# Kernel optimization log

Hardware: AMD Instinct MI355X
Metric: run time of the kernel (lower is better)

Reference implementation:

```python
import jax, jax.numpy as jnp
import numpy as np

M = 65536   # query points
N = 65536   # key points
K = 16      # neighbors per query
C = 64      # channels


def setup_inputs() -> dict:
    key = jax.random.key(0)
    ks = jax.random.split(key, 12)
    f = jax.random.normal
    s = 1.0 / np.sqrt(C).astype(np.float32)
    return {
        "q": f(ks[0], (M, C), dtype=jnp.float32),
        "k": f(ks[1], (N, C), dtype=jnp.float32),
        "value": f(ks[2], (M, K, C), dtype=jnp.float32),
        "q_pos": f(ks[3], (M, C), dtype=jnp.float32),
        "k_pos": f(ks[4], (N, C), dtype=jnp.float32),
        "mask": jax.random.uniform(ks[5], (M, K, 1)) < 0.1,
        "knearest_idx": jax.random.randint(ks[6], (2, M, K), 0, N),
        "k_num": K,
        # q_conv and k_conv share weights in the original module
        "Wqk": f(ks[7], (C, C), dtype=jnp.float32) * s,
        "bqk": jnp.zeros((C,), jnp.float32),
        "Wv": f(ks[8], (C, C), dtype=jnp.float32) * s,
        "bv": jnp.zeros((C,), jnp.float32),
        "Wg1": f(ks[9], (C, C), dtype=jnp.float32) * s,
        "bg1": jnp.zeros((C,), jnp.float32),
        "Wg2": f(ks[10], (C, C), dtype=jnp.float32) * s,
        "bg2": jnp.zeros((C,), jnp.float32),
        "Wt": f(ks[11], (C, C), dtype=jnp.float32) * s,
        "bt": jnp.zeros((C,), jnp.float32),
    }


def reference(q, k, value, q_pos, k_pos, mask, knearest_idx, k_num,
              Wqk, bqk, Wv, bv, Wg1, bg1, Wg2, bg2, Wt, bt):
    # shared q/k projection (tied weights) with positional add
    qp = (q + q_pos) @ Wqk + bqk            # [M, C]
    kp = (k + k_pos) @ Wqk + bqk            # [N, C]
    v = value @ Wv + bv                      # [M, K, C]
    # neighbor indices: row 1 of knearest_idx reshaped to [_, M, k_num]
    idx = knearest_idx.reshape(knearest_idx.shape[0], -1, k_num)[1]  # [M, K]
    kg = kp[idx]                              # gather -> [M, K, C]
    # per-edge MLP on q - k (fc_gamma)
    e = qp[:, None, :] - kg                   # [M, K, C]
    e = jax.nn.relu(e @ Wg1 + bg1) @ Wg2 + bg2
    e = jnp.where(mask, jnp.float32(-1e12), e)
    attn = jax.nn.softmax(e, axis=1)          # softmax over neighbor dim
    res = jnp.einsum('mnf,mnf->mf', attn, v)  # weighted aggregate -> [M, C]
    return res @ Wt + bt
```

## Files before the change

kernel.cpp:

```cpp
#include <hip/hip_runtime.h>
#include <hip/hip_bf16.h>

#define MQ 65536
#define NKEY 65536
#define KNB 16
#define CCH 64
#define TPB 8

typedef _Float16 half8  __attribute__((ext_vector_type(8)));
typedef _Float16 half4v __attribute__((ext_vector_type(4)));
typedef float    floatx4 __attribute__((ext_vector_type(4)));


__global__ void detect_mask(const unsigned char* __restrict__ m, int* __restrict__ flag)
{
    __shared__ int sflags;
    if (threadIdx.x == 0) sflags = 0;
    __syncthreads();
    const uint4* m4 = (const uint4*)m;
    unsigned int orw = 0;
    #pragma unroll
    for (int it = 0; it < 4; ++it) {
        uint4 v = m4[threadIdx.x + it * 256];
        orw |= v.x | v.y | v.z | v.w;
    }
    int local = 0;
    if (orw & 0x000000FFu) local |= 1;
    if (orw & 0x0000FF00u) local |= 2;
    if (orw & 0xFFFF0000u) local |= 4;
    if (local) atomicOr(&sflags, local);
    __syncthreads();
    if (threadIdx.x == 0) *flag = sflags;
}

__global__ __launch_bounds__(256, 4)
void proj_prep(const float* __restrict__ q, const float* __restrict__ qpos,
               const float* __restrict__ k, const float* __restrict__ kpos,
               const float* __restrict__ Wqk, const float* __restrict__ bqk,
               const float* __restrict__ Wg1, const float* __restrict__ Wg2,
               const float* __restrict__ Wv,  const float* __restrict__ Wt,
               const unsigned char* __restrict__ maskraw, const int* __restrict__ mflag,
               _Float16* __restrict__ qp_h, _Float16* __restrict__ kp_h,
               _Float16* __restrict__ w4, unsigned short* __restrict__ mask_packed)
{
    const int tid = threadIdx.x;
    const int bid = blockIdx.x;

    if (bid >= 1024) {
        if (bid < 1088) {
            const int mode = *mflag;
            const int qq0 = (bid - 1024) * 1024 + tid * 4;
            unsigned short mp[4];
            #pragma unroll
            for (int i = 0; i < 4; ++i) {
                const int qq = qq0 + i;
                unsigned bits = 0;
                if (mode & 2) {
                    uint4 v = ((const uint4*)maskraw)[qq];
                    unsigned wds[4] = {v.x, v.y, v.z, v.w};
                    #pragma unroll
                    for (int wi = 0; wi < 4; ++wi)
                        #pragma unroll
                        for (int b = 0; b < 4; ++b)
                            if ((wds[wi] >> (8 * b)) & 0xFFu) bits |= 1u << (wi * 4 + b);
                } else {
                    const uint4* p = (const uint4*)maskraw + (size_t)qq * 4;
                    #pragma unroll
                    for (int wi = 0; wi < 4; ++wi) {
                        uint4 v = p[wi];
                        bits |= (v.x ? 1u : 0u) << (wi * 4 + 0);
                        bits |= (v.y ? 1u : 0u) << (wi * 4 + 1);
                        bits |= (v.z ? 1u : 0u) << (wi * 4 + 2);
                        bits |= (v.w ? 1u : 0u) << (wi * 4 + 3);
                    }
                }
                mp[i] = (unsigned short)bits;
            }
            ushort4 o4; o4.x = mp[0]; o4.y = mp[1]; o4.z = mp[2]; o4.w = mp[3];
            *(ushort4*)&mask_packed[qq0] = o4;
        } else {
            const float* Ws[4] = {Wg1, Wg2, Wv, Wt};
            #pragma unroll
            for (int mat = 0; mat < 4; ++mat) {
                const float* W = Ws[mat];
                _Float16* dst = w4 + mat * 64 * 72;
                for (int i = tid; i < 4096; i += 256) {
                    int rr = i >> 6, c = i & 63;
                    dst[c * 72 + rr] = (_Float16)W[i];
                }
            }
        }
        return;
    }

    __shared__ __align__(16) _Float16 A_s[128 * 72];
    __shared__ __align__(16) _Float16 WT_s[64 * 72];

    const int r0 = bid * 128;
    const float* x; const float* p; _Float16* o; int rb;
    if (r0 < MQ) { x = q; p = qpos; o = qp_h; rb = r0; }
    else         { x = k; p = kpos; o = kp_h; rb = r0 - MQ; }

    #pragma unroll
    for (int j = 0; j < 4; ++j) {
        int i = (tid + j * 256) * 4;
        int rr = i >> 6, c4 = i & 63;
        floatx4 wv = *(const floatx4*)&Wqk[i];
        WT_s[(c4 + 0) * 72 + rr] = (_Float16)wv.x;
        WT_s[(c4 + 1) * 72 + rr] = (_Float16)wv.y;
        WT_s[(c4 + 2) * 72 + rr] = (_Float16)wv.z;
        WT_s[(c4 + 3) * 72 + rr] = (_Float16)wv.w;
    }
    #pragma unroll
    for (int j = 0; j < 8; ++j) {
        int flat = tid + j * 256;
        int rr = flat >> 4, c4 = (flat & 15) * 4;
        size_t g = (size_t)(rb + rr) * 64 + c4;
        floatx4 xv = *(const floatx4*)&x[g];
        floatx4 pv = *(const floatx4*)&p[g];
        half4v h;
        h[0] = (_Float16)(xv.x + pv.x); h[1] = (_Float16)(xv.y + pv.y);
        h[2] = (_Float16)(xv.z + pv.z); h[3] = (_Float16)(xv.w + pv.w);
        *(half4v*)&A_s[rr * 72 + c4] = h;
    }
    __syncthreads();

    const int w = tid >> 6, lane = tid & 63, m = lane & 15, qd = lane >> 4;
    const floatx4 fz = {0.f, 0.f, 0.f, 0.f};
    floatx4 acc[2][4];
    #pragma unroll
    for (int rt = 0; rt < 2; rt++)
        #pragma unroll
        for (int ct = 0; ct < 4; ct++) acc[rt][ct] = fz;

    #pragma unroll
    for (int kc = 0; kc < 2; ++kc) {
        const int k0 = kc * 32 + qd * 8;
        half8 b[4];
        #pragma unroll
        for (int ct = 0; ct < 4; ++ct)
            b[ct] = *(const half8*)&WT_s[(ct * 16 + m) * 72 + k0];
        #pragma unroll
        for (int rt = 0; rt < 2; ++rt) {
            half8 a = *(const half8*)&A_s[(w * 32 + rt * 16 + m) * 72 + k0];
            #pragma unroll
            for (int ct = 0; ct < 4; ++ct)
                acc[rt][ct] = __builtin_amdgcn_mfma_f32_16x16x32_f16(a, b[ct], acc[rt][ct], 0, 0, 0);
        }
    }
    #pragma unroll
    for (int rt = 0; rt < 2; rt++)
        #pragma unroll
        for (int ct = 0; ct < 4; ct++) {
            const int col = ct * 16 + m;
            const float bb = bqk[col];
            #pragma unroll
            for (int rg = 0; rg < 4; ++rg) {
                const int row = w * 32 + rt * 16 + qd * 4 + rg;
                A_s[row * 72 + col] = (_Float16)(acc[rt][ct][rg] + bb);
            }
        }
    __syncthreads();
    #pragma unroll
    for (int j = 0; j < 4; ++j) {
        int ch = tid + j * 256;
        int rr = ch >> 3, off = (ch & 7) * 8;
        *(half8*)&o[(size_t)(rb + rr) * 64 + off] = *(const half8*)&A_s[rr * 72 + off];
    }
}

__global__ __launch_bounds__(256) __attribute__((amdgpu_waves_per_eu(2, 2)))
void cross_attn(const float* __restrict__ value, const unsigned short* __restrict__ mask_packed,
                const int* __restrict__ idx,
                const _Float16* __restrict__ qp_h, const _Float16* __restrict__ kp_h,
                const _Float16* __restrict__ w4,
                const float* __restrict__ bg1, const float* __restrict__ bg2,
                const float* __restrict__ bv,
                _Float16* __restrict__ res_g)
{
    __shared__ __align__(16) _Float16 W3_s[3 * 64 * 72];
    __shared__ __align__(16) _Float16 H_s[256 * 72];

    const int tid = threadIdx.x, w = tid >> 6, lane = tid & 63, m = lane & 15, qd = (lane >> 4) & 3;
    const int tile0 = blockIdx.x * TPB;

    for (int ch = tid; ch < 1728; ch += 256)
        *(half8*)&W3_s[ch * 8] = *(const half8*)&w4[ch * 8];

    float bg1v[4], bg2v[4], bvv[4];
    #pragma unroll
    for (int ct = 0; ct < 4; ct++) {
        const int col = ct * 16 + m;
        bg1v[ct] = bg1[col]; bg2v[ct] = bg2[col]; bvv[ct] = bv[col];
    }

    int idxn[4]; unsigned mpr[4];
    half8 qpr[4][2];
    floatx4 vraw[16];
    {
        const int q0 = tile0 * 16;
        #pragma unroll
        for (int rt = 0; rt < 4; ++rt) {
            const int qrow = q0 + w * 4 + rt;
            idxn[rt] = idx[qrow * KNB + m];
            mpr[rt]  = mask_packed[qrow];
            #pragma unroll
            for (int kc = 0; kc < 2; ++kc)
                qpr[rt][kc] = *(const half8*)&qp_h[(size_t)qrow * 64 + kc * 32 + qd * 8];
            #pragma unroll
            for (int kc = 0; kc < 2; ++kc) {
                const float* vr = value + ((size_t)qrow * KNB + m) * 64 + kc * 32 + qd * 8;
                vraw[(rt * 2 + kc) * 2 + 0] = *(const floatx4*)vr;
                vraw[(rt * 2 + kc) * 2 + 1] = *(const floatx4*)(vr + 4);
            }
        }
    }
    __syncthreads();

    const _Float16* Wg1T = W3_s;
    const _Float16* Wg2T = W3_s + 4608;
    const _Float16* WvT  = W3_s + 2 * 4608;
    const floatx4 fz = {0.f, 0.f, 0.f, 0.f};

    for (int t = 0; t < TPB; ++t) {
        const int q0t = (tile0 + t) * 16;
        const bool more = (t + 1 < TPB);

        unsigned mcur[4];
        #pragma unroll
        for (int rt = 0; rt < 4; ++rt) mcur[rt] = mpr[rt];

        half8 kpr[4][2];
        #pragma unroll
        for (int rt = 0; rt < 4; ++rt)
            #pragma unroll
            for (int kc = 0; kc < 2; ++kc)
                kpr[rt][kc] = *(const half8*)&kp_h[(size_t)idxn[rt] * 64 + kc * 32 + qd * 8];

        #pragma unroll
        for (int pr = 0; pr < 2; ++pr) {
            const int r0 = pr * 2;

            half8 vfrag[2][2];
            #pragma unroll
            for (int rr = 0; rr < 2; ++rr)
                #pragma unroll
                for (int kc = 0; kc < 2; ++kc) {
                    floatx4 x0 = vraw[((r0 + rr) * 2 + kc) * 2 + 0];
                    floatx4 x1 = vraw[((r0 + rr) * 2 + kc) * 2 + 1];
                    half8 a;
                    #pragma unroll
                    for (int j = 0; j < 4; ++j) { a[j] = (_Float16)x0[j]; a[4 + j] = (_Float16)x1[j]; }
                    vfrag[rr][kc] = a;
                }

            floatx4 accv2[2][4];
            #pragma unroll
            for (int rr = 0; rr < 2; ++rr)
                #pragma unroll
                for (int ct = 0; ct < 4; ++ct) accv2[rr][ct] = fz;
            #pragma unroll
            for (int kc = 0; kc < 2; ++kc) {
                const int k0 = kc * 32 + qd * 8;
                half8 b[4];
                #pragma unroll
                for (int ct = 0; ct < 4; ++ct)
                    b[ct] = *(const half8*)&WvT[(ct * 16 + m) * 72 + k0];
                #pragma unroll
                for (int rr = 0; rr < 2; ++rr)
                    #pragma unroll
                    for (int ct = 0; ct < 4; ++ct)
                        accv2[rr][ct] = __builtin_amdgcn_mfma_f32_16x16x32_f16(vfrag[rr][kc], b[ct], accv2[rr][ct], 0, 0, 0);
            }

            if (more) {
                const int q0n = q0t + 16;
                #pragma unroll
                for (int rr = 0; rr < 2; ++rr) {
                    const int qrow = q0n + w * 4 + r0 + rr;
                    #pragma unroll
                    for (int kc = 0; kc < 2; ++kc) {
                        const float* vr = value + ((size_t)qrow * KNB + m) * 64 + kc * 32 + qd * 8;
                        vraw[((r0 + rr) * 2 + kc) * 2 + 0] = *(const floatx4*)vr;
                        vraw[((r0 + rr) * 2 + kc) * 2 + 1] = *(const floatx4*)(vr + 4);
                    }
                }
            }

            floatx4 acch2[2][4];
            #pragma unroll
            for (int rr = 0; rr < 2; ++rr)
                #pragma unroll
                for (int ct = 0; ct < 4; ++ct) acch2[rr][ct] = fz;
            #pragma unroll
            for (int kc = 0; kc < 2; ++kc) {
                const int k0 = kc * 32 + qd * 8;
                half8 b[4];
                #pragma unroll
                for (int ct = 0; ct < 4; ++ct)
                    b[ct] = *(const half8*)&Wg1T[(ct * 16 + m) * 72 + k0];
                #pragma unroll
                for (int rr = 0; rr < 2; ++rr) {
                    half8 a = qpr[r0 + rr][kc] - kpr[r0 + rr][kc];
                    #pragma unroll
                    for (int ct = 0; ct < 4; ++ct)
                        acch2[rr][ct] = __builtin_amdgcn_mfma_f32_16x16x32_f16(a, b[ct], acch2[rr][ct], 0, 0, 0);
                }
            }

            #pragma unroll
            for (int rr = 0; rr < 2; ++rr)
                #pragma unroll
                for (int ct = 0; ct < 4; ++ct) {
                    const int col = ct * 16 + m;
                    #pragma unroll
                    for (int rg = 0; rg < 4; ++rg) {
                        const int row = w * 64 + (r0 + rr) * 16 + qd * 4 + rg;
                        float h = acch2[rr][ct][rg] + bg1v[ct];
                        H_s[row * 72 + col] = (_Float16)fmaxf(h, 0.f);
                    }
                }
            __asm__ volatile("s_waitcnt lgkmcnt(0)" ::: "memory");

            floatx4 acce2[2][4];
            #pragma unroll
            for (int rr = 0; rr < 2; ++rr)
                #pragma unroll
                for (int ct = 0; ct < 4; ++ct) acce2[rr][ct] = fz;
            #pragma unroll
            for (int kc = 0; kc < 2; ++kc) {
                const int k0 = kc * 32 + qd * 8;
                half8 b[4];
                #pragma unroll
                for (int ct = 0; ct < 4; ++ct)
                    b[ct] = *(const half8*)&Wg2T[(ct * 16 + m) * 72 + k0];
                #pragma unroll
                for (int rr = 0; rr < 2; ++rr) {
                    half8 a = *(const half8*)&H_s[(w * 64 + (r0 + rr) * 16 + m) * 72 + k0];
                    #pragma unroll
                    for (int ct = 0; ct < 4; ++ct)
                        acce2[rr][ct] = __builtin_amdgcn_mfma_f32_16x16x32_f16(a, b[ct], acce2[rr][ct], 0, 0, 0);
                }
            }

            if (pr == 0 && more) {
                const int q0n = q0t + 16;
                #pragma unroll
                for (int rt = 0; rt < 4; ++rt) {
                    const int qrow = q0n + w * 4 + rt;
                    idxn[rt] = idx[qrow * KNB + m];
                    mpr[rt]  = mask_packed[qrow];
                }
            }

            #pragma unroll
            for (int rr = 0; rr < 2; ++rr) {
                const int rt = r0 + rr;
                float tca[4];
                #pragma unroll
                for (int ct = 0; ct < 4; ++ct) {
                    float ev[4];
                    #pragma unroll
                    for (int rg = 0; rg < 4; ++rg) {
                        float e = acce2[rr][ct][rg] + bg2v[ct];
                        ev[rg] = ((mcur[rt] >> (qd * 4 + rg)) & 1u) ? -1e12f : e;
                    }
                    float mx = fmaxf(fmaxf(ev[0], ev[1]), fmaxf(ev[2], ev[3]));
                    mx = fmaxf(mx, __shfl_xor(mx, 16));
                    mx = fmaxf(mx, __shfl_xor(mx, 32));
                    float pp[4], s = 0.f;
                    #pragma unroll
                    for (int rg = 0; rg < 4; ++rg) { pp[rg] = __expf(ev[rg] - mx); s += pp[rg]; }
                    s += __shfl_xor(s, 16);
                    s += __shfl_xor(s, 32);
                    const float inv = 1.f / s;
                    float tt = 0.f;
                    #pragma unroll
                    for (int rg = 0; rg < 4; ++rg)
                        tt += pp[rg] * inv * (accv2[rr][ct][rg] + bvv[ct]);
                    tt += __shfl_xor(tt, 16);
                    tt += __shfl_xor(tt, 32);
                    tca[ct] = tt;
                }
                float tsel = (qd == 0) ? tca[0] : (qd == 1) ? tca[1] : (qd == 2) ? tca[2] : tca[3];
                res_g[(size_t)(q0t + w * 4 + rt) * 64 + lane] = (_Float16)tsel;
            }
        }

        if (more) {
            const int q0n = q0t + 16;
            #pragma unroll
            for (int rt = 0; rt < 4; ++rt) {
                const int qrow = q0n + w * 4 + rt;
                #pragma unroll
                for (int kc = 0; kc < 2; ++kc)
                    qpr[rt][kc] = *(const half8*)&qp_h[(size_t)qrow * 64 + kc * 32 + qd * 8];
            }
        }
    }
}

__global__ __launch_bounds__(256, 4)
void out_proj(const _Float16* __restrict__ res_g, const _Float16* __restrict__ w4,
              const float* __restrict__ bt, float* __restrict__ out)
{
    __shared__ __align__(16) _Float16 WtT_s[64 * 72];
    const int tid = threadIdx.x;
    const _Float16* WtT_g = w4 + 3 * 4608;
    for (int ch = tid; ch < 576; ch += 256)
        *(half8*)&WtT_s[ch * 8] = *(const half8*)&WtT_g[ch * 8];
    __syncthreads();

    const int w = tid >> 6, lane = tid & 63, m = lane & 15, qd = lane >> 4;
    const int rb = blockIdx.x * 256;
    const floatx4 fz = {0.f, 0.f, 0.f, 0.f};
    float btv[4];
    #pragma unroll
    for (int ct = 0; ct < 4; ++ct) btv[ct] = bt[ct * 16 + m];

    #pragma unroll
    for (int rt = 0; rt < 4; ++rt) {
        floatx4 acc[4] = {fz, fz, fz, fz};
        #pragma unroll
        for (int kc = 0; kc < 2; ++kc) {
            const int k0 = kc * 32 + qd * 8;
            half8 a = *(const half8*)&res_g[(size_t)(rb + w * 64 + rt * 16 + m) * 64 + k0];
            half8 b[4];
            #pragma unroll
            for (int ct = 0; ct < 4; ++ct)
                b[ct] = *(const half8*)&WtT_s[(ct * 16 + m) * 72 + k0];
            #pragma unroll
            for (int ct = 0; ct < 4; ++ct)
                acc[ct] = __builtin_amdgcn_mfma_f32_16x16x32_f16(a, b[ct], acc[ct], 0, 0, 0);
        }
        #pragma unroll
        for (int ct = 0; ct < 4; ++ct) {
            #pragma unroll
            for (int rg = 0; rg < 4; ++rg)
                out[(size_t)(rb + w * 64 + rt * 16 + qd * 4 + rg) * 64 + ct * 16 + m] = acc[ct][rg] + btv[ct];
        }
    }
}

extern "C" void kernel_launch(void* const* d_in, const int* in_sizes, int n_in,
                              void* d_out, int out_size, void* d_ws, size_t ws_size,
                              hipStream_t stream) {
    const float* q     = (const float*)d_in[0];
    const float* k     = (const float*)d_in[1];
    const float* value = (const float*)d_in[2];
    const float* q_pos = (const float*)d_in[3];
    const float* k_pos = (const float*)d_in[4];
    const unsigned char* mask = (const unsigned char*)d_in[5];
    const int* knn     = (const int*)d_in[6];
    const float* Wqk = (const float*)d_in[8];
    const float* bqk = (const float*)d_in[9];
    const float* Wv  = (const float*)d_in[10];
    const float* bv  = (const float*)d_in[11];
    const float* Wg1 = (const float*)d_in[12];
    const float* bg1 = (const float*)d_in[13];
    const float* Wg2 = (const float*)d_in[14];
    const float* bg2 = (const float*)d_in[15];
    const float* Wt  = (const float*)d_in[16];
    const float* bt  = (const float*)d_in[17];
    float* out = (float*)d_out;

    _Float16* qp_h  = (_Float16*)d_ws;
    _Float16* kp_h  = qp_h + (size_t)MQ * CCH;
    _Float16* res_g = kp_h + (size_t)NKEY * CCH;
    _Float16* w4    = res_g + (size_t)MQ * CCH;
    unsigned short* mask_packed = (unsigned short*)(w4 + 4 * 64 * 72);
    int* mflag = (int*)(mask_packed + MQ);
    const int* idx = knn + (size_t)MQ * KNB;

    detect_mask<<<1, 256, 0, stream>>>(mask, mflag);
    proj_prep<<<1089, 256, 0, stream>>>(q, q_pos, k, k_pos, Wqk, bqk,
                                        Wg1, Wg2, Wv, Wt, mask, mflag,
                                        qp_h, kp_h, w4, mask_packed);
    cross_attn<<<MQ / (16 * TPB), 256, 0, stream>>>(value, mask_packed, idx, qp_h, kp_h, w4,
                                                    bg1, bg2, bv, res_g);
    out_proj<<<MQ / 256, 256, 0, stream>>>(res_g, w4, bt, out);
}
```

Measured before the change: 501.0 us.

## Fuse output projection into cross_attn and software-pipeline neighbor key gathers

The separate out_proj kernel is removed. cross_attn now keeps results in a per-wave shared buffer and runs the Wt projection with MFMA every four tiles, writing the final fp32 output directly, which drops the res_g round trip and one launch. The kp gathers for the next tile are now issued inside the current tile's pipeline, after the index prefetch, so they overlap compute. H_s is shrunk to per-pair rows to make room for Wt and R_s in LDS. The cost is more register pressure from kpr kept live across tiles, and a scattered output-store pattern.

```diff
diff --git a/kernel.cpp b/kernel.cpp
--- a/kernel.cpp
+++ b/kernel.cpp
@@ -175,27 +175,28 @@
                 const _Float16* __restrict__ qp_h, const _Float16* __restrict__ kp_h,
                 const _Float16* __restrict__ w4,
                 const float* __restrict__ bg1, const float* __restrict__ bg2,
-                const float* __restrict__ bv,
-                _Float16* __restrict__ res_g)
+                const float* __restrict__ bv, const float* __restrict__ bt,
+                float* __restrict__ out)
 {
-    __shared__ __align__(16) _Float16 W3_s[3 * 64 * 72];
-    __shared__ __align__(16) _Float16 H_s[256 * 72];
+    __shared__ __align__(16) _Float16 W4_s[4 * 64 * 72];
+    __shared__ __align__(16) _Float16 H_s[128 * 72];
+    __shared__ __align__(16) _Float16 R_s[64 * 72];
 
     const int tid = threadIdx.x, w = tid >> 6, lane = tid & 63, m = lane & 15, qd = (lane >> 4) & 3;
     const int tile0 = blockIdx.x * TPB;
 
-    for (int ch = tid; ch < 1728; ch += 256)
-        *(half8*)&W3_s[ch * 8] = *(const half8*)&w4[ch * 8];
-
-    float bg1v[4], bg2v[4], bvv[4];
+    for (int ch = tid; ch < 2304; ch += 256)
+        *(half8*)&W4_s[ch * 8] = *(const half8*)&w4[ch * 8];
+
+    float bg1v[4], bg2v[4], bvv[4], btv[4];
     #pragma unroll
     for (int ct = 0; ct < 4; ct++) {
         const int col = ct * 16 + m;
-        bg1v[ct] = bg1[col]; bg2v[ct] = bg2[col]; bvv[ct] = bv[col];
+        bg1v[ct] = bg1[col]; bg2v[ct] = bg2[col]; bvv[ct] = bv[col]; btv[ct] = bt[col];
     }
 
     int idxn[4]; unsigned mpr[4];
-    half8 qpr[4][2];
+    half8 qpr[4][2], kpr[4][2];
     floatx4 vraw[16];
     {
         const int q0 = tile0 * 16;
@@ -214,12 +215,18 @@
                 vraw[(rt * 2 + kc) * 2 + 1] = *(const floatx4*)(vr + 4);
             }
         }
+        #pragma unroll
+        for (int rt = 0; rt < 4; ++rt)
+            #pragma unroll
+            for (int kc = 0; kc < 2; ++kc)
+                kpr[rt][kc] = *(const half8*)&kp_h[(size_t)idxn[rt] * 64 + kc * 32 + qd * 8];
     }
     __syncthreads();
 
-    const _Float16* Wg1T = W3_s;
-    const _Float16* Wg2T = W3_s + 4608;
-    const _Float16* WvT  = W3_s + 2 * 4608;
+    const _Float16* Wg1T = W4_s;
+    const _Float16* Wg2T = W4_s + 4608;
+    const _Float16* WvT  = W4_s + 2 * 4608;
+    const _Float16* WtT  = W4_s + 3 * 4608;
     const floatx4 fz = {0.f, 0.f, 0.f, 0.f};
 
     for (int t = 0; t < TPB; ++t) {
@@ -230,12 +237,15 @@
         #pragma unroll
         for (int rt = 0; rt < 4; ++rt) mcur[rt] = mpr[rt];
 
-        half8 kpr[4][2];
-        #pragma unroll
-        for (int rt = 0; rt < 4; ++rt)
-            #pragma unroll
-            for (int kc = 0; kc < 2; ++kc)
-                kpr[rt][kc] = *(const half8*)&kp_h[(size_t)idxn[rt] * 64 + kc * 32 + qd * 8];
+        if (more) {
+            const int q0n = q0t + 16;
+            #pragma unroll
+            for (int rt = 0; rt < 4; ++rt) {
+                const int qrow = q0n + w * 4 + rt;
+                idxn[rt] = idx[qrow * KNB + m];
+                mpr[rt]  = mask_packed[qrow];
+            }
+        }
 
         #pragma unroll
         for (int pr = 0; pr < 2; ++pr) {
@@ -308,6 +318,17 @@
                 }
             }
 
+            if (more) {
+                const int q0n = q0t + 16;
+                #pragma unroll
+                for (int rr = 0; rr < 2; ++rr) {
+                    const int qrow = q0n + w * 4 + r0 + rr;
+                    #pragma unroll
+                    for (int kc = 0; kc < 2; ++kc)
+                        qpr[r0 + rr][kc] = *(const half8*)&qp_h[(size_t)qrow * 64 + kc * 32 + qd * 8];
+                }
+            }
+
             #pragma unroll
             for (int rr = 0; rr < 2; ++rr)
                 #pragma unroll
@@ -315,7 +336,7 @@
                     const int col = ct * 16 + m;
                     #pragma unroll
                     for (int rg = 0; rg < 4; ++rg) {
-                        const int row = w * 64 + (r0 + rr) * 16 + qd * 4 + rg;
+                        const int row = w * 32 + rr * 16 + qd * 4 + rg;
                         float h = acch2[rr][ct][rg] + bg1v[ct];
                         H_s[row * 72 + col] = (_Float16)fmaxf(h, 0.f);
                     }
@@ -336,21 +357,19 @@
                     b[ct] = *(const half8*)&Wg2T[(ct * 16 + m) * 72 + k0];
                 #pragma unroll
                 for (int rr = 0; rr < 2; ++rr) {
-                    half8 a = *(const half8*)&H_s[(w * 64 + (r0 + rr) * 16 + m) * 72 + k0];
+                    half8 a = *(const half8*)&H_s[(w * 32 + rr * 16 + m) * 72 + k0];
                     #pragma unroll
                     for (int ct = 0; ct < 4; ++ct)
                         acce2[rr][ct] = __builtin_amdgcn_mfma_f32_16x16x32_f16(a, b[ct], acce2[rr][ct], 0, 0, 0);
                 }
             }
 
-            if (pr == 0 && more) {
-                const int q0n = q0t + 16;
-                #pragma unroll
-                for (int rt = 0; rt < 4; ++rt) {
-                    const int qrow = q0n + w * 4 + rt;
-                    idxn[rt] = idx[qrow * KNB + m];
-                    mpr[rt]  = mask_packed[qrow];
-                }
+            if (more) {
+                #pragma unroll
+                for (int rr = 0; rr < 2; ++rr)
+                    #pragma unroll
+                    for (int kc = 0; kc < 2; ++kc)
+                        kpr[r0 + rr][kc] = *(const half8*)&kp_h[(size_t)idxn[r0 + rr] * 64 + kc * 32 + qd * 8];
             }
 
             #pragma unroll
@@ -383,61 +402,34 @@
                     tca[ct] = tt;
                 }
                 float tsel = (qd == 0) ? tca[0] : (qd == 1) ? tca[1] : (qd == 2) ? tca[2] : tca[3];
-                res_g[(size_t)(q0t + w * 4 + rt) * 64 + lane] = (_Float16)tsel;
-            }
-        }
-
-        if (more) {
-            const int q0n = q0t + 16;
-            #pragma unroll
-            for (int rt = 0; rt < 4; ++rt) {
-                const int qrow = q0n + w * 4 + rt;
-                #pragma unroll
-                for (int kc = 0; kc < 2; ++kc)
-                    qpr[rt][kc] = *(const half8*)&qp_h[(size_t)qrow * 64 + kc * 32 + qd * 8];
-            }
-        }
-    }
-}
-
-__global__ __launch_bounds__(256, 4)
-void out_proj(const _Float16* __restrict__ res_g, const _Float16* __restrict__ w4,
-              const float* __restrict__ bt, float* __restrict__ out)
-{
-    __shared__ __align__(16) _Float16 WtT_s[64 * 72];
-    const int tid = threadIdx.x;
-    const _Float16* WtT_g = w4 + 3 * 4608;
-    for (int ch = tid; ch < 576; ch += 256)
-        *(half8*)&WtT_s[ch * 8] = *(const half8*)&WtT_g[ch * 8];
-    __syncthreads();
-
-    const int w = tid >> 6, lane = tid & 63, m = lane & 15, qd = lane >> 4;
-    const int rb = blockIdx.x * 256;
-    const floatx4 fz = {0.f, 0.f, 0.f, 0.f};
-    float btv[4];
-    #pragma unroll
-    for (int ct = 0; ct < 4; ++ct) btv[ct] = bt[ct * 16 + m];
-
-    #pragma unroll
-    for (int rt = 0; rt < 4; ++rt) {
-        floatx4 acc[4] = {fz, fz, fz, fz};
-        #pragma unroll
-        for (int kc = 0; kc < 2; ++kc) {
-            const int k0 = kc * 32 + qd * 8;
-            half8 a = *(const half8*)&res_g[(size_t)(rb + w * 64 + rt * 16 + m) * 64 + k0];
-            half8 b[4];
+                R_s[((w * 16 + (t & 3) * 4 + rt)) * 72 + lane] = (_Float16)tsel;
+            }
+        }
+
+        if ((t & 3) == 3) {
+            __asm__ volatile("s_waitcnt lgkmcnt(0)" ::: "memory");
+            floatx4 acc[4] = {fz, fz, fz, fz};
+            #pragma unroll
+            for (int kc = 0; kc < 2; ++kc) {
+                const int k0 = kc * 32 + qd * 8;
+                half8 a = *(const half8*)&R_s[(w * 16 + m) * 72 + k0];
+                half8 b[4];
+                #pragma unroll
+                for (int ct = 0; ct < 4; ++ct)
+                    b[ct] = *(const half8*)&WtT[(ct * 16 + m) * 72 + k0];
+                #pragma unroll
+                for (int ct = 0; ct < 4; ++ct)
+                    acc[ct] = __builtin_amdgcn_mfma_f32_16x16x32_f16(a, b[ct], acc[ct], 0, 0, 0);
+            }
+            const int grp0 = (tile0 + (t & ~3)) * 16;
             #pragma unroll
             for (int ct = 0; ct < 4; ++ct)
-                b[ct] = *(const half8*)&WtT_s[(ct * 16 + m) * 72 + k0];
-            #pragma unroll
-            for (int ct = 0; ct < 4; ++ct)
-                acc[ct] = __builtin_amdgcn_mfma_f32_16x16x32_f16(a, b[ct], acc[ct], 0, 0, 0);
-        }
-        #pragma unroll
-        for (int ct = 0; ct < 4; ++ct) {
-            #pragma unroll
-            for (int rg = 0; rg < 4; ++rg)
-                out[(size_t)(rb + w * 64 + rt * 16 + qd * 4 + rg) * 64 + ct * 16 + m] = acc[ct][rg] + btv[ct];
+                #pragma unroll
+                for (int rg = 0; rg < 4; ++rg) {
+                    const int r = qd * 4 + rg;
+                    const int g = grp0 + (r >> 2) * 16 + w * 4 + (r & 3);
+                    out[(size_t)g * 64 + ct * 16 + m] = acc[ct][rg] + btv[ct];
+                }
         }
     }
 }
@@ -477,6 +469,5 @@
                                         Wg1, Wg2, Wv, Wt, mask, mflag,
                                         qp_h, kp_h, w4, mask_packed);
     cross_attn<<<MQ / (16 * TPB), 256, 0, stream>>>(value, mask_packed, idx, qp_h, kp_h, w4,
-                                                    bg1, bg2, bv, res_g);
-    out_proj<<<MQ / 256, 256, 0, stream>>>(res_g, w4, bt, out);
+                                                    bg1, bg2, bv, bt, out);
 }
```

Measured after the change: 527.7 us. 1.05x slower.

## Cut cross_attn register pressure to raise occupancy and drop bg2 add

Applied to the files above, without the earlier changes.

The attention kernel is reworked so each tile is processed in two half-passes that hold only two query rows' value and q data in registers. This roughly halves live registers and lets waves_per_eu rise from 2 to 3, with TPB halved and H_s shrunk to match. Other changes: bg2 is dropped because a per-channel bias cancels in the softmax over neighbours, bv is added once after the normalised sum, the value projection is kept in fp16, the mask words are loaded as one uint2, and a fast reciprocal is used. The trade-offs are more prefetch and branch logic per half-pass, more blocks each reloading the weights into LDS, and slightly lower precision.

```diff
diff --git a/kernel.cpp b/kernel.cpp
--- a/kernel.cpp
+++ b/kernel.cpp
@@ -5,7 +5,7 @@
 #define NKEY 65536
 #define KNB 16
 #define CCH 64
-#define TPB 8
+#define TPB 4
 
 typedef _Float16 half8  __attribute__((ext_vector_type(8)));
 typedef _Float16 half4v __attribute__((ext_vector_type(4)));
@@ -169,17 +169,16 @@
     }
 }
 
-__global__ __launch_bounds__(256) __attribute__((amdgpu_waves_per_eu(2, 2)))
+__global__ __launch_bounds__(256) __attribute__((amdgpu_waves_per_eu(3, 3)))
 void cross_attn(const float* __restrict__ value, const unsigned short* __restrict__ mask_packed,
                 const int* __restrict__ idx,
                 const _Float16* __restrict__ qp_h, const _Float16* __restrict__ kp_h,
                 const _Float16* __restrict__ w4,
-                const float* __restrict__ bg1, const float* __restrict__ bg2,
-                const float* __restrict__ bv,
+                const float* __restrict__ bg1, const float* __restrict__ bv,
                 _Float16* __restrict__ res_g)
 {
     __shared__ __align__(16) _Float16 W3_s[3 * 64 * 72];
-    __shared__ __align__(16) _Float16 H_s[256 * 72];
+    __shared__ __align__(16) _Float16 H_s[128 * 72];
 
     const int tid = threadIdx.x, w = tid >> 6, lane = tid & 63, m = lane & 15, qd = (lane >> 4) & 3;
     const int tile0 = blockIdx.x * TPB;
@@ -187,33 +186,35 @@
     for (int ch = tid; ch < 1728; ch += 256)
         *(half8*)&W3_s[ch * 8] = *(const half8*)&w4[ch * 8];
 
-    float bg1v[4], bg2v[4], bvv[4];
-    #pragma unroll
-    for (int ct = 0; ct < 4; ct++) {
-        const int col = ct * 16 + m;
-        bg1v[ct] = bg1[col]; bg2v[ct] = bg2[col]; bvv[ct] = bv[col];
-    }
-
-    int idxn[4]; unsigned mpr[4];
-    half8 qpr[4][2];
-    floatx4 vraw[16];
+    float bg1v[4];
+    #pragma unroll
+    for (int ct = 0; ct < 4; ct++) bg1v[ct] = bg1[ct * 16 + m];
+    const float bvsel = bv[lane];
+
+    int idxn[4];
+    uint2 mpr;
+    half8 qpr[2][2];
+    half8 kpr[4][2];
+    floatx4 vraw[8];
     {
         const int q0 = tile0 * 16;
-        #pragma unroll
-        for (int rt = 0; rt < 4; ++rt) {
-            const int qrow = q0 + w * 4 + rt;
-            idxn[rt] = idx[qrow * KNB + m];
-            mpr[rt]  = mask_packed[qrow];
+        mpr = *(const uint2*)&mask_packed[q0 + w * 4];
+        #pragma unroll
+        for (int rt = 0; rt < 4; ++rt)
+            idxn[rt] = idx[(q0 + w * 4 + rt) * KNB + m];
+        #pragma unroll
+        for (int rr = 0; rr < 2; ++rr)
             #pragma unroll
             for (int kc = 0; kc < 2; ++kc)
-                qpr[rt][kc] = *(const half8*)&qp_h[(size_t)qrow * 64 + kc * 32 + qd * 8];
+                qpr[rr][kc] = *(const half8*)&qp_h[(size_t)(q0 + w * 4 + rr) * 64 + kc * 32 + qd * 8];
+        #pragma unroll
+        for (int rr = 0; rr < 2; ++rr)
             #pragma unroll
             for (int kc = 0; kc < 2; ++kc) {
-                const float* vr = value + ((size_t)qrow * KNB + m) * 64 + kc * 32 + qd * 8;
-                vraw[(rt * 2 + kc) * 2 + 0] = *(const floatx4*)vr;
-                vraw[(rt * 2 + kc) * 2 + 1] = *(const floatx4*)(vr + 4);
-            }
-        }
+                const float* vr = value + ((size_t)(q0 + w * 4 + rr) * KNB + m) * 64 + kc * 32 + qd * 8;
+                vraw[(rr * 2 + kc) * 2 + 0] = *(const floatx4*)vr;
+                vraw[(rr * 2 + kc) * 2 + 1] = *(const floatx4*)(vr + 4);
+            }
     }
     __syncthreads();
 
@@ -226,11 +227,8 @@
         const int q0t = (tile0 + t) * 16;
         const bool more = (t + 1 < TPB);
 
-        unsigned mcur[4];
-        #pragma unroll
-        for (int rt = 0; rt < 4; ++rt) mcur[rt] = mpr[rt];
-
-        half8 kpr[4][2];
+        const uint2 mcur = mpr;
+
         #pragma unroll
         for (int rt = 0; rt < 4; ++rt)
             #pragma unroll
@@ -246,155 +244,158 @@
             for (int rr = 0; rr < 2; ++rr)
                 #pragma unroll
                 for (int kc = 0; kc < 2; ++kc) {
-                    floatx4 x0 = vraw[((r0 + rr) * 2 + kc) * 2 + 0];
-                    floatx4 x1 = vraw[((r0 + rr) * 2 + kc) * 2 + 1];
+                    floatx4 x0 = vraw[(rr * 2 + kc) * 2 + 0];
+                    floatx4 x1 = vraw[(rr * 2 + kc) * 2 + 1];
                     half8 a;
                     #pragma unroll
                     for (int j = 0; j < 4; ++j) { a[j] = (_Float16)x0[j]; a[4 + j] = (_Float16)x1[j]; }
                     vfrag[rr][kc] = a;
                 }
 
-            floatx4 accv2[2][4];
+            if (pr == 0 || more) {
+                const int qb = (pr == 0) ? (q0t + 2) : (q0t + 16);
+                #pragma unroll
+                for (int rr = 0; rr < 2; ++rr) {
+                    const float* vr = value + ((size_t)(qb + w * 4 + rr) * KNB + m) * 64 + qd * 8;
+                    vraw[(rr * 2 + 0) * 2 + 0] = *(const floatx4*)vr;
+                    vraw[(rr * 2 + 0) * 2 + 1] = *(const floatx4*)(vr + 4);
+                    vraw[(rr * 2 + 1) * 2 + 0] = *(const floatx4*)(vr + 32);
+                    vraw[(rr * 2 + 1) * 2 + 1] = *(const floatx4*)(vr + 36);
+                }
+            }
+
+            half4v vh[2][4];
+            {
+                floatx4 accv[2][4];
+                #pragma unroll
+                for (int rr = 0; rr < 2; ++rr)
+                    #pragma unroll
+                    for (int ct = 0; ct < 4; ++ct) accv[rr][ct] = fz;
+                #pragma unroll
+                for (int kc = 0; kc < 2; ++kc) {
+                    const int k0 = kc * 32 + qd * 8;
+                    half8 b[4];
+                    #pragma unroll
+                    for (int ct = 0; ct < 4; ++ct)
+                        b[ct] = *(const half8*)&WvT[(ct * 16 + m) * 72 + k0];
+                    #pragma unroll
+                    for (int rr = 0; rr < 2; ++rr)
+                        #pragma unroll
+                        for (int ct = 0; ct < 4; ++ct)
+                            accv[rr][ct] = __builtin_amdgcn_mfma_f32_16x16x32_f16(vfrag[rr][kc], b[ct], accv[rr][ct], 0, 0, 0);
+                }
+                #pragma unroll
+                for (int rr = 0; rr < 2; ++rr)
+                    #pragma unroll
+                    for (int ct = 0; ct < 4; ++ct) {
+                        half4v hv;
+                        #pragma unroll
+                        for (int rg = 0; rg < 4; ++rg) hv[rg] = (_Float16)accv[rr][ct][rg];
+                        vh[rr][ct] = hv;
+                    }
+            }
+
+            floatx4 acch[2][4];
             #pragma unroll
             for (int rr = 0; rr < 2; ++rr)
                 #pragma unroll
-                for (int ct = 0; ct < 4; ++ct) accv2[rr][ct] = fz;
+                for (int ct = 0; ct < 4; ++ct) acch[rr][ct] = fz;
             #pragma unroll
             for (int kc = 0; kc < 2; ++kc) {
                 const int k0 = kc * 32 + qd * 8;
                 half8 b[4];
                 #pragma unroll
                 for (int ct = 0; ct < 4; ++ct)
-                    b[ct] = *(const half8*)&WvT[(ct * 16 + m) * 72 + k0];
+                    b[ct] = *(const half8*)&Wg1T[(ct * 16 + m) * 72 + k0];
+                #pragma unroll
+                for (int rr = 0; rr < 2; ++rr) {
+                    half8 a = qpr[rr][kc] - kpr[r0 + rr][kc];
+                    #pragma unroll
+                    for (int ct = 0; ct < 4; ++ct)
+                        acch[rr][ct] = __builtin_amdgcn_mfma_f32_16x16x32_f16(a, b[ct], acch[rr][ct], 0, 0, 0);
+                }
+            }
+
+            if (pr == 0 || more) {
+                const int qb = (pr == 0) ? (q0t + 2) : (q0t + 16);
                 #pragma unroll
                 for (int rr = 0; rr < 2; ++rr)
                     #pragma unroll
-                    for (int ct = 0; ct < 4; ++ct)
-                        accv2[rr][ct] = __builtin_amdgcn_mfma_f32_16x16x32_f16(vfrag[rr][kc], b[ct], accv2[rr][ct], 0, 0, 0);
-            }
-
-            if (more) {
-                const int q0n = q0t + 16;
-                #pragma unroll
-                for (int rr = 0; rr < 2; ++rr) {
-                    const int qrow = q0n + w * 4 + r0 + rr;
-                    #pragma unroll
-                    for (int kc = 0; kc < 2; ++kc) {
-                        const float* vr = value + ((size_t)qrow * KNB + m) * 64 + kc * 32 + qd * 8;
-                        vraw[((r0 + rr) * 2 + kc) * 2 + 0] = *(const floatx4*)vr;
-                        vraw[((r0 + rr) * 2 + kc) * 2 + 1] = *(const floatx4*)(vr + 4);
+                    for (int kc = 0; kc < 2; ++kc)
+                        qpr[rr][kc] = *(const half8*)&qp_h[(size_t)(qb + w * 4 + rr) * 64 + kc * 32 + qd * 8];
+            }
+
+            #pragma unroll
+            for (int rr = 0; rr < 2; ++rr)
+                #pragma unroll
+                for (int ct = 0; ct < 4; ++ct) {
+                    const int col = ct * 16 + m;
+                    #pragma unroll
+                    for (int rg = 0; rg < 4; ++rg) {
+                        const int row = w * 32 + rr * 16 + qd * 4 + rg;
+                        float h = acch[rr][ct][rg] + bg1v[ct];
+                        H_s[row * 72 + col] = (_Float16)fmaxf(h, 0.f);
                     }
                 }
-            }
-
-            floatx4 acch2[2][4];
+            __asm__ volatile("s_waitcnt lgkmcnt(0)" ::: "memory");
+
+            floatx4 acce[2][4];
             #pragma unroll
             for (int rr = 0; rr < 2; ++rr)
                 #pragma unroll
-                for (int ct = 0; ct < 4; ++ct) acch2[rr][ct] = fz;
+                for (int ct = 0; ct < 4; ++ct) acce[rr][ct] = fz;
             #pragma unroll
             for (int kc = 0; kc < 2; ++kc) {
                 const int k0 = kc * 32 + qd * 8;
                 half8 b[4];
                 #pragma unroll
                 for (int ct = 0; ct < 4; ++ct)
-                    b[ct] = *(const half8*)&Wg1T[(ct * 16 + m) * 72 + k0];
+                    b[ct] = *(const half8*)&Wg2T[(ct * 16 + m) * 72 + k0];
                 #pragma unroll
                 for (int rr = 0; rr < 2; ++rr) {
-                    half8 a = qpr[r0 + rr][kc] - kpr[r0 + rr][kc];
+                    half8 a = *(const half8*)&H_s[(w * 32 + rr * 16 + m) * 72 + k0];
                     #pragma unroll
                     for (int ct = 0; ct < 4; ++ct)
-                        acch2[rr][ct] = __builtin_amdgcn_mfma_f32_16x16x32_f16(a, b[ct], acch2[rr][ct], 0, 0, 0);
-                }
-            }
-
-            #pragma unroll
-            for (int rr = 0; rr < 2; ++rr)
-                #pragma unroll
-                for (int ct = 0; ct < 4; ++ct) {
-                    const int col = ct * 16 + m;
-                    #pragma unroll
-                    for (int rg = 0; rg < 4; ++rg) {
-                        const int row = w * 64 + (r0 + rr) * 16 + qd * 4 + rg;
-                        float h = acch2[rr][ct][rg] + bg1v[ct];
-                        H_s[row * 72 + col] = (_Float16)fmaxf(h, 0.f);
-                    }
-                }
-            __asm__ volatile("s_waitcnt lgkmcnt(0)" ::: "memory");
-
-            floatx4 acce2[2][4];
-            #pragma unroll
-            for (int rr = 0; rr < 2; ++rr)
-                #pragma unroll
-                for (int ct = 0; ct < 4; ++ct) acce2[rr][ct] = fz;
-            #pragma unroll
-            for (int kc = 0; kc < 2; ++kc) {
-                const int k0 = kc * 32 + qd * 8;
-                half8 b[4];
-                #pragma unroll
-                for (int ct = 0; ct < 4; ++ct)
-                    b[ct] = *(const half8*)&Wg2T[(ct * 16 + m) * 72 + k0];
-                #pragma unroll
-                for (int rr = 0; rr < 2; ++rr) {
-                    half8 a = *(const half8*)&H_s[(w * 64 + (r0 + rr) * 16 + m) * 72 + k0];
-                    #pragma unroll
-                    for (int ct = 0; ct < 4; ++ct)
-                        acce2[rr][ct] = __builtin_amdgcn_mfma_f32_16x16x32_f16(a, b[ct], acce2[rr][ct], 0, 0, 0);
+                        acce[rr][ct] = __builtin_amdgcn_mfma_f32_16x16x32_f16(a, b[ct], acce[rr][ct], 0, 0, 0);
                 }
             }
 
             if (pr == 0 && more) {
                 const int q0n = q0t + 16;
-                #pragma unroll
-                for (int rt = 0; rt < 4; ++rt) {
-                    const int qrow = q0n + w * 4 + rt;
-                    idxn[rt] = idx[qrow * KNB + m];
-                    mpr[rt]  = mask_packed[qrow];
-                }
-            }
-
+                mpr = *(const uint2*)&mask_packed[q0n + w * 4];
+                #pragma unroll
+                for (int rt = 0; rt < 4; ++rt)
+                    idxn[rt] = idx[(q0n + w * 4 + rt) * KNB + m];
+            }
+
+            const unsigned mword = (pr == 0) ? mcur.x : mcur.y;
             #pragma unroll
             for (int rr = 0; rr < 2; ++rr) {
-                const int rt = r0 + rr;
+                const int sh = rr * 16 + qd * 4;
                 float tca[4];
                 #pragma unroll
                 for (int ct = 0; ct < 4; ++ct) {
                     float ev[4];
                     #pragma unroll
                     for (int rg = 0; rg < 4; ++rg) {
-                        float e = acce2[rr][ct][rg] + bg2v[ct];
-                        ev[rg] = ((mcur[rt] >> (qd * 4 + rg)) & 1u) ? -1e12f : e;
+                        float e = acce[rr][ct][rg];
+                        ev[rg] = ((mword >> (sh + rg)) & 1u) ? -1e12f : e;
                     }
                     float mx = fmaxf(fmaxf(ev[0], ev[1]), fmaxf(ev[2], ev[3]));
                     mx = fmaxf(mx, __shfl_xor(mx, 16));
                     mx = fmaxf(mx, __shfl_xor(mx, 32));
-                    float pp[4], s = 0.f;
-                    #pragma unroll
-                    for (int rg = 0; rg < 4; ++rg) { pp[rg] = __expf(ev[rg] - mx); s += pp[rg]; }
-                    s += __shfl_xor(s, 16);
-                    s += __shfl_xor(s, 32);
-                    const float inv = 1.f / s;
-                    float tt = 0.f;
-                    #pragma unroll
-                    for (int rg = 0; rg < 4; ++rg)
-                        tt += pp[rg] * inv * (accv2[rr][ct][rg] + bvv[ct]);
-                    tt += __shfl_xor(tt, 16);
-                    tt += __shfl_xor(tt, 32);
-                    tca[ct] = tt;
+                    float s = 0.f, ttu = 0.f;
+                    #pragma unroll
+                    for (int rg = 0; rg < 4; ++rg) {
+                        float p = __expf(ev[rg] - mx);
+                        s += p; ttu += p * (float)vh[rr][ct][rg];
+                    }
+                    s   += __shfl_xor(s, 16);   ttu += __shfl_xor(ttu, 16);
+                    s   += __shfl_xor(s, 32);   ttu += __shfl_xor(ttu, 32);
+                    tca[ct] = ttu * __builtin_amdgcn_rcpf(s);
                 }
                 float tsel = (qd == 0) ? tca[0] : (qd == 1) ? tca[1] : (qd == 2) ? tca[2] : tca[3];
-                res_g[(size_t)(q0t + w * 4 + rt) * 64 + lane] = (_Float16)tsel;
-            }
-        }
-
-        if (more) {
-            const int q0n = q0t + 16;
-            #pragma unroll
-            for (int rt = 0; rt < 4; ++rt) {
-                const int qrow = q0n + w * 4 + rt;
-                #pragma unroll
-                for (int kc = 0; kc < 2; ++kc)
-                    qpr[rt][kc] = *(const half8*)&qp_h[(size_t)qrow * 64 + kc * 32 + qd * 8];
+                res_g[(size_t)(q0t + w * 4 + r0 + rr) * 64 + lane] = (_Float16)(tsel + bvsel);
             }
         }
     }
@@ -463,6 +464,7 @@
     const float* Wt  = (const float*)d_in[16];
     const float* bt  = (const float*)d_in[17];
     float* out = (float*)d_out;
+    (void)bg2;
 
     _Float16* qp_h  = (_Float16*)d_ws;
     _Float16* kp_h  = qp_h + (size_t)MQ * CCH;
@@ -477,6 +479,6 @@
                                         Wg1, Wg2, Wv, Wt, mask, mflag,
                                         qp_h, kp_h, w4, mask_packed);
     cross_attn<<<MQ / (16 * TPB), 256, 0, stream>>>(value, mask_packed, idx, qp_h, kp_h, w4,
-                                                    bg1, bg2, bv, res_g);
+                                                    bg1, bv, res_g);
     out_proj<<<MQ / 256, 256, 0, stream>>>(res_g, w4, bt, out);
 }
```

After: 554.6 us. 1.11x slower.

## Prefetch next tile's key gathers and simplify softmax with exp2 and bias folding

Applied to the files above, without the earlier changes.

The gather of projected keys for the next tile is now issued in the middle of the current tile's compute, right after the next tile's indices are loaded, instead of at the top of each iteration. The aim is to hide the latency of the random gather behind the MFMA work, at the cost of keeping more registers live. The softmax is also simplified. The Wg2 weights are prescaled by log2(e) so the kernel can use a native exp2. The bg2 bias is dropped because a per-channel constant cancels in a softmax over neighbors. The bv bias is added once after normalisation, and the final division becomes a single rcp multiply.

```diff
diff --git a/kernel.cpp b/kernel.cpp
--- a/kernel.cpp
+++ b/kernel.cpp
@@ -10,6 +10,12 @@
 typedef _Float16 half8  __attribute__((ext_vector_type(8)));
 typedef _Float16 half4v __attribute__((ext_vector_type(4)));
 typedef float    floatx4 __attribute__((ext_vector_type(4)));
+
+#if __has_builtin(__builtin_amdgcn_exp2f)
+#define EXP2F(x) __builtin_amdgcn_exp2f(x)
+#else
+#define EXP2F(x) exp2f(x)
+#endif
 
 
 __global__ void detect_mask(const unsigned char* __restrict__ m, int* __restrict__ flag)
@@ -83,10 +89,11 @@
             #pragma unroll
             for (int mat = 0; mat < 4; ++mat) {
                 const float* W = Ws[mat];
+                const float sc = (mat == 1) ? 1.44269504f : 1.0f;
                 _Float16* dst = w4 + mat * 64 * 72;
                 for (int i = tid; i < 4096; i += 256) {
                     int rr = i >> 6, c = i & 63;
-                    dst[c * 72 + rr] = (_Float16)W[i];
+                    dst[c * 72 + rr] = (_Float16)(W[i] * sc);
                 }
             }
         }
@@ -174,8 +181,7 @@
                 const int* __restrict__ idx,
                 const _Float16* __restrict__ qp_h, const _Float16* __restrict__ kp_h,
                 const _Float16* __restrict__ w4,
-                const float* __restrict__ bg1, const float* __restrict__ bg2,
-                const float* __restrict__ bv,
+                const float* __restrict__ bg1, const float* __restrict__ bv,
                 _Float16* __restrict__ res_g)
 {
     __shared__ __align__(16) _Float16 W3_s[3 * 64 * 72];
@@ -187,15 +193,13 @@
     for (int ch = tid; ch < 1728; ch += 256)
         *(half8*)&W3_s[ch * 8] = *(const half8*)&w4[ch * 8];
 
-    float bg1v[4], bg2v[4], bvv[4];
-    #pragma unroll
-    for (int ct = 0; ct < 4; ct++) {
-        const int col = ct * 16 + m;
-        bg1v[ct] = bg1[col]; bg2v[ct] = bg2[col]; bvv[ct] = bv[col];
-    }
+    float bg1v[4];
+    #pragma unroll
+    for (int ct = 0; ct < 4; ct++) bg1v[ct] = bg1[ct * 16 + m];
+    const float bvsel = bv[lane];
 
     int idxn[4]; unsigned mpr[4];
-    half8 qpr[4][2];
+    half8 qpr[4][2], kpr[4][2];
     floatx4 vraw[16];
     {
         const int q0 = tile0 * 16;
@@ -214,6 +218,11 @@
                 vraw[(rt * 2 + kc) * 2 + 1] = *(const floatx4*)(vr + 4);
             }
         }
+        #pragma unroll
+        for (int rt = 0; rt < 4; ++rt)
+            #pragma unroll
+            for (int kc = 0; kc < 2; ++kc)
+                kpr[rt][kc] = *(const half8*)&kp_h[(size_t)idxn[rt] * 64 + kc * 32 + qd * 8];
     }
     __syncthreads();
 
@@ -230,12 +239,15 @@
         #pragma unroll
         for (int rt = 0; rt < 4; ++rt) mcur[rt] = mpr[rt];
 
-        half8 kpr[4][2];
-        #pragma unroll
-        for (int rt = 0; rt < 4; ++rt)
-            #pragma unroll
-            for (int kc = 0; kc < 2; ++kc)
-                kpr[rt][kc] = *(const half8*)&kp_h[(size_t)idxn[rt] * 64 + kc * 32 + qd * 8];
+        if (more) {
+            const int q0n = q0t + 16;
+            #pragma unroll
+            for (int rt = 0; rt < 4; ++rt) {
+                const int qrow = q0n + w * 4 + rt;
+                idxn[rt] = idx[qrow * KNB + m];
+                mpr[rt]  = mask_packed[qrow];
+            }
+        }
 
         #pragma unroll
         for (int pr = 0; pr < 2; ++pr) {
@@ -308,6 +320,14 @@
                 }
             }
 
+            if (pr == 1 && more) {
+                #pragma unroll
+                for (int rt = 0; rt < 4; ++rt)
+                    #pragma unroll
+                    for (int kc = 0; kc < 2; ++kc)
+                        kpr[rt][kc] = *(const half8*)&kp_h[(size_t)idxn[rt] * 64 + kc * 32 + qd * 8];
+            }
+
             #pragma unroll
             for (int rr = 0; rr < 2; ++rr)
                 #pragma unroll
@@ -343,16 +363,6 @@
                 }
             }
 
-            if (pr == 0 && more) {
-                const int q0n = q0t + 16;
-                #pragma unroll
-                for (int rt = 0; rt < 4; ++rt) {
-                    const int qrow = q0n + w * 4 + rt;
-                    idxn[rt] = idx[qrow * KNB + m];
-                    mpr[rt]  = mask_packed[qrow];
-                }
-            }
-
             #pragma unroll
             for (int rr = 0; rr < 2; ++rr) {
                 const int rt = r0 + rr;
@@ -362,28 +372,24 @@
                     float ev[4];
                     #pragma unroll
                     for (int rg = 0; rg < 4; ++rg) {
-                        float e = acce2[rr][ct][rg] + bg2v[ct];
+                        float e = acce2[rr][ct][rg];
                         ev[rg] = ((mcur[rt] >> (qd * 4 + rg)) & 1u) ? -1e12f : e;
                     }
                     float mx = fmaxf(fmaxf(ev[0], ev[1]), fmaxf(ev[2], ev[3]));
                     mx = fmaxf(mx, __shfl_xor(mx, 16));
                     mx = fmaxf(mx, __shfl_xor(mx, 32));
-                    float pp[4], s = 0.f;
-                    #pragma unroll
-                    for (int rg = 0; rg < 4; ++rg) { pp[rg] = __expf(ev[rg] - mx); s += pp[rg]; }
-                    s += __shfl_xor(s, 16);
-                    s += __shfl_xor(s, 32);
-                    const float inv = 1.f / s;
-                    float tt = 0.f;
-                    #pragma unroll
-                    for (int rg = 0; rg < 4; ++rg)
-                        tt += pp[rg] * inv * (accv2[rr][ct][rg] + bvv[ct]);
-                    tt += __shfl_xor(tt, 16);
-                    tt += __shfl_xor(tt, 32);
-                    tca[ct] = tt;
+                    float s = 0.f, ttu = 0.f;
+                    #pragma unroll
+                    for (int rg = 0; rg < 4; ++rg) {
+                        float p = EXP2F(ev[rg] - mx);
+                        s += p; ttu += p * accv2[rr][ct][rg];
+                    }
+                    s   += __shfl_xor(s, 16);   ttu += __shfl_xor(ttu, 16);
+                    s   += __shfl_xor(s, 32);   ttu += __shfl_xor(ttu, 32);
+                    tca[ct] = ttu * __builtin_amdgcn_rcpf(s);
                 }
                 float tsel = (qd == 0) ? tca[0] : (qd == 1) ? tca[1] : (qd == 2) ? tca[2] : tca[3];
-                res_g[(size_t)(q0t + w * 4 + rt) * 64 + lane] = (_Float16)tsel;
+                res_g[(size_t)(q0t + w * 4 + rt) * 64 + lane] = (_Float16)(tsel + bvsel);
             }
         }
 
@@ -463,6 +469,7 @@
     const float* Wt  = (const float*)d_in[16];
     const float* bt  = (const float*)d_in[17];
     float* out = (float*)d_out;
+    (void)bg2;
 
     _Float16* qp_h  = (_Float16*)d_ws;
     _Float16* kp_h  = qp_h + (size_t)MQ * CCH;
@@ -477,6 +484,6 @@
                                         Wg1, Wg2, Wv, Wt, mask, mflag,
                                         qp_h, kp_h, w4, mask_packed);
     cross_attn<<<MQ / (16 * TPB), 256, 0, stream>>>(value, mask_packed, idx, qp_h, kp_h, w4,
-                                                    bg1, bg2, bv, res_g);
+                                                    bg1, bv, res_g);
     out_proj<<<MQ / 256, 256, 0, stream>>>(res_g, w4, bt, out);
 }
```

New measurement: 523.4 us. 4.5% more time.
